# Optimization experiments

Hardware: AMD Instinct MI355X
Metric: run time of the kernel (lower is better)

## Reference

```python
import jax, jax.numpy as jnp
import numpy as np

B, D, G, K, U = 8192, 4096, 256, 32, 64


def setup_inputs() -> dict:
    key = jax.random.key(0)
    kx, kw, ki = jax.random.split(key, 3)
    x = jax.random.normal(kx, (B, D), dtype=jnp.float32)
    # per-group kernels stacked: group g has kernel [K, U]
    kernels = jax.random.normal(kw, (G, K, U), dtype=jnp.float32) * 0.02
    bias = jnp.zeros((U,), dtype=jnp.float32)
    # uniform-size index groups (TF version: list of G index lists of len K)
    indices = jax.random.randint(ki, (G, K), 0, D, dtype=jnp.int32)
    return {"x": x, "kernels": kernels, "bias": bias, "indices": indices}


def reference(x, kernels, bias, indices):
    # gather feature subsets for every group at once: [B, G, K]
    sel = x[:, indices]
    # grouped small matmuls, concatenated on group axis: [B, G, U]
    out = jnp.einsum('bgk,gku->bgu', sel, kernels)
    out = out + bias  # bias broadcast over last axis (tf.nn.bias_add)
    return jax.nn.relu(out)
```

## Files before the change

kernel.cpp:

```cpp
#include <hip/hip_runtime.h>
#include <hip/hip_bf16.h>


#define B_ 8192
#define D_ 4096
#define G_ 256
#define K_ 32
#define U_ 64
#define QG 8

typedef short v8s __attribute__((ext_vector_type(8)));
typedef float f32x4 __attribute__((ext_vector_type(4)));

__device__ __forceinline__ unsigned short f2bf(float f) {
    unsigned int u = __float_as_uint(f);
    u = (u + 0x7FFFu + ((u >> 16) & 1u)) >> 16;
    return (unsigned short)u;
}

__global__ void prep_kb(const float* __restrict__ kern, unsigned short* __restrict__ kb) {
    int tid = blockIdx.x * blockDim.x + threadIdx.x;
    if (tid >= G_ * K_ * U_) return;
    int u = tid & (U_ - 1);
    int k = (tid >> 6) & (K_ - 1);
    int g = tid >> 11;
    int t = u & 3;
    int col = u >> 2;
    int lane = ((k >> 3) << 4) | col;
    int j = k & 7;
    kb[((((g << 2) + t) << 6 | lane) << 3) | j] = f2bf(kern[tid]);
}

#define XS 4100

__global__ void __launch_bounds__(512) sdense(
        const float* __restrict__ x, const unsigned short* __restrict__ kb,
        const float* __restrict__ bias, const int* __restrict__ idx,
        float* __restrict__ out) {
    extern __shared__ unsigned short lx[];
    const int tid = threadIdx.x;
    const int b0 = blockIdx.x << 4;
    const int lane = tid & 63;
    const int w = tid >> 6;

    {
        const int row = (w << 1) + (lane >> 5);
        const int l32 = lane & 31;
        const float* xr = x + (size_t)(b0 + row) * D_;
        unsigned short* lr = lx + row * XS;
        #pragma unroll
        for (int i = 0; i < 16; ++i) {
            int col = (i << 8) + (l32 << 3);
            float4 v0 = *(const float4*)(xr + col);
            float4 v1 = *(const float4*)(xr + col + 4);
            union { unsigned short u[8]; v8s v; } st;
            st.u[0] = f2bf(v0.x); st.u[1] = f2bf(v0.y);
            st.u[2] = f2bf(v0.z); st.u[3] = f2bf(v0.w);
            st.u[4] = f2bf(v1.x); st.u[5] = f2bf(v1.y);
            st.u[6] = f2bf(v1.z); st.u[7] = f2bf(v1.w);
            *(v8s*)(lr + col) = st.v;
        }
    }
    __syncthreads();

    const int grp = lane >> 4;
    const int l15 = lane & 15;
    const int rowb = l15 * XS;
    const int kk0 = grp << 3;

    const float4 bias_v = *(const float4*)(bias + (l15 << 2));

    const v8s* kbv = (const v8s*)kb;

    for (int q = 0; q < 4; ++q) {
        const int g0 = (q << 6) + (w << 3);

        f32x4 acc[QG][4];
        #pragma unroll
        for (int j = 0; j < QG; ++j) {
            const int g = g0 + j;
            const int4* ip = (const int4*)(idx + (g << 5) + kk0);
            int4 ia = ip[0], ib = ip[1];
            const v8s* kg = kbv + (g << 8) + lane;
            v8s k0 = kg[0], k1 = kg[64], k2 = kg[128], k3 = kg[192];

            union { unsigned short u[8]; v8s v; } A;
            A.u[0] = lx[rowb + ia.x]; A.u[1] = lx[rowb + ia.y];
            A.u[2] = lx[rowb + ia.z]; A.u[3] = lx[rowb + ia.w];
            A.u[4] = lx[rowb + ib.x]; A.u[5] = lx[rowb + ib.y];
            A.u[6] = lx[rowb + ib.z]; A.u[7] = lx[rowb + ib.w];

            f32x4 z = {0.f, 0.f, 0.f, 0.f};
            acc[j][0] = __builtin_amdgcn_mfma_f32_16x16x32_bf16(A.v, k0, z, 0, 0, 0);
            acc[j][1] = __builtin_amdgcn_mfma_f32_16x16x32_bf16(A.v, k1, z, 0, 0, 0);
            acc[j][2] = __builtin_amdgcn_mfma_f32_16x16x32_bf16(A.v, k2, z, 0, 0, 0);
            acc[j][3] = __builtin_amdgcn_mfma_f32_16x16x32_bf16(A.v, k3, z, 0, 0, 0);
        }

        #pragma unroll
        for (int r = 0; r < 4; ++r) {
            float* obr = out + (size_t)(b0 + (grp << 2) + r) * (G_ * U_)
                             + (g0 << 6) + (l15 << 2);
            #pragma unroll
            for (int j = 0; j < QG; ++j) {
                float4 v;
                v.x = acc[j][0][r] + bias_v.x;
                v.y = acc[j][1][r] + bias_v.y;
                v.z = acc[j][2][r] + bias_v.z;
                v.w = acc[j][3][r] + bias_v.w;
                v.x = v.x > 0.f ? v.x : 0.f;
                v.y = v.y > 0.f ? v.y : 0.f;
                v.z = v.z > 0.f ? v.z : 0.f;
                v.w = v.w > 0.f ? v.w : 0.f;
                *(float4*)(obr + (j << 6)) = v;
            }
        }

        __builtin_amdgcn_s_barrier();
    }
}

extern "C" void kernel_launch(void* const* d_in, const int* in_sizes, int n_in,
                              void* d_out, int out_size, void* d_ws, size_t ws_size,
                              hipStream_t stream) {
    const float* x    = (const float*)d_in[0];
    const float* kern = (const float*)d_in[1];
    const float* bias = (const float*)d_in[2];
    const int*   idx  = (const int*)d_in[3];
    float* out = (float*)d_out;
    unsigned short* kb = (unsigned short*)d_ws;

    prep_kb<<<(G_ * K_ * U_ + 255) / 256, 256, 0, stream>>>(kern, kb);
    sdense<<<B_ / 16, 512, 16 * XS * sizeof(unsigned short), stream>>>(x, kb, bias, idx, out);
}
```

Baseline: 169.9 us.

## Double-buffer kernel/index loads, process two row tiles per block with swizzled mapping

```diff
diff --git a/kernel.cpp b/kernel.cpp
--- a/kernel.cpp
+++ b/kernel.cpp
@@ -7,7 +7,7 @@
 #define G_ 256
 #define K_ 32
 #define U_ 64
-#define QG 8
+#define QG 4
 
 typedef short v8s __attribute__((ext_vector_type(8)));
 typedef float f32x4 __attribute__((ext_vector_type(4)));
@@ -33,90 +33,109 @@
 
 #define XS 4100
 
+#define LOADS(BANK, G0)                                                   \
+    _Pragma("unroll")                                                     \
+    for (int j = 0; j < QG; ++j) {                                        \
+        const int4* ip = (const int4*)(idx + (((G0) + j) << 5) + kk0);    \
+        pia[BANK][j] = ip[0]; pib[BANK][j] = ip[1];                       \
+        const v8s* kg = kbv + (((G0) + j) << 8) + lane;                   \
+        pk[BANK][j][0] = kg[0];   pk[BANK][j][1] = kg[64];                \
+        pk[BANK][j][2] = kg[128]; pk[BANK][j][3] = kg[192];               \
+    }
+
+#define STEP(CB, NB, Q)                                                   \
+    {                                                                     \
+        const int g0 = ((Q) << 5) + (w << 2);                             \
+               \
+        LOADS(NB, (((((Q) + 1) & 7) << 5) + (w << 2)));                   \
+        f32x4 acc[QG][4];                                                 \
+        _Pragma("unroll")                                                 \
+        for (int j = 0; j < QG; ++j) {                                    \
+            union { unsigned short u[8]; v8s v; } A;                      \
+            A.u[0] = lx[rowb + pia[CB][j].x];                             \
+            A.u[1] = lx[rowb + pia[CB][j].y];                             \
+            A.u[2] = lx[rowb + pia[CB][j].z];                             \
+            A.u[3] = lx[rowb + pia[CB][j].w];                             \
+            A.u[4] = lx[rowb + pib[CB][j].x];                             \
+            A.u[5] = lx[rowb + pib[CB][j].y];                             \
+            A.u[6] = lx[rowb + pib[CB][j].z];                             \
+            A.u[7] = lx[rowb + pib[CB][j].w];                             \
+            f32x4 z = {0.f, 0.f, 0.f, 0.f};                               \
+            acc[j][0] = __builtin_amdgcn_mfma_f32_16x16x32_bf16(A.v, pk[CB][j][0], z, 0, 0, 0); \
+            acc[j][1] = __builtin_amdgcn_mfma_f32_16x16x32_bf16(A.v, pk[CB][j][1], z, 0, 0, 0); \
+            acc[j][2] = __builtin_amdgcn_mfma_f32_16x16x32_bf16(A.v, pk[CB][j][2], z, 0, 0, 0); \
+            acc[j][3] = __builtin_amdgcn_mfma_f32_16x16x32_bf16(A.v, pk[CB][j][3], z, 0, 0, 0); \
+        }                                                                 \
+        _Pragma("unroll")                                                 \
+        for (int r = 0; r < 4; ++r) {                                     \
+            float* obr = out + (size_t)(b0 + (grp << 2) + r) * (G_ * U_)  \
+                             + (g0 << 6) + (l15 << 2);                    \
+            _Pragma("unroll")                                             \
+            for (int j = 0; j < QG; ++j) {                                \
+                float4 v;                                                 \
+                v.x = acc[j][0][r] + bias_v.x;                            \
+                v.y = acc[j][1][r] + bias_v.y;                            \
+                v.z = acc[j][2][r] + bias_v.z;                            \
+                v.w = acc[j][3][r] + bias_v.w;                            \
+                v.x = v.x > 0.f ? v.x : 0.f;                              \
+                v.y = v.y > 0.f ? v.y : 0.f;                              \
+                v.z = v.z > 0.f ? v.z : 0.f;                              \
+                v.w = v.w > 0.f ? v.w : 0.f;                              \
+                *(float4*)(obr + (j << 6)) = v;                           \
+            }                                                             \
+        }                                                                 \
+        __builtin_amdgcn_s_barrier();                                     \
+    }
+
 __global__ void __launch_bounds__(512) sdense(
         const float* __restrict__ x, const unsigned short* __restrict__ kb,
         const float* __restrict__ bias, const int* __restrict__ idx,
         float* __restrict__ out) {
     extern __shared__ unsigned short lx[];
     const int tid = threadIdx.x;
-    const int b0 = blockIdx.x << 4;
     const int lane = tid & 63;
     const int w = tid >> 6;
-
-    {
-        const int row = (w << 1) + (lane >> 5);
-        const int l32 = lane & 31;
-        const float* xr = x + (size_t)(b0 + row) * D_;
-        unsigned short* lr = lx + row * XS;
-        #pragma unroll
-        for (int i = 0; i < 16; ++i) {
-            int col = (i << 8) + (l32 << 3);
-            float4 v0 = *(const float4*)(xr + col);
-            float4 v1 = *(const float4*)(xr + col + 4);
-            union { unsigned short u[8]; v8s v; } st;
-            st.u[0] = f2bf(v0.x); st.u[1] = f2bf(v0.y);
-            st.u[2] = f2bf(v0.z); st.u[3] = f2bf(v0.w);
-            st.u[4] = f2bf(v1.x); st.u[5] = f2bf(v1.y);
-            st.u[6] = f2bf(v1.z); st.u[7] = f2bf(v1.w);
-            *(v8s*)(lr + col) = st.v;
-        }
-    }
-    __syncthreads();
+    const int tile = ((blockIdx.x & 7) << 5) | (blockIdx.x >> 3);
 
     const int grp = lane >> 4;
     const int l15 = lane & 15;
     const int rowb = l15 * XS;
     const int kk0 = grp << 3;
-
     const float4 bias_v = *(const float4*)(bias + (l15 << 2));
-
     const v8s* kbv = (const v8s*)kb;
 
-    for (int q = 0; q < 4; ++q) {
-        const int g0 = (q << 6) + (w << 3);
+    int4 pia[2][QG], pib[2][QG];
+    v8s pk[2][QG][4];
 
-        f32x4 acc[QG][4];
-        #pragma unroll
-        for (int j = 0; j < QG; ++j) {
-            const int g = g0 + j;
-            const int4* ip = (const int4*)(idx + (g << 5) + kk0);
-            int4 ia = ip[0], ib = ip[1];
-            const v8s* kg = kbv + (g << 8) + lane;
-            v8s k0 = kg[0], k1 = kg[64], k2 = kg[128], k3 = kg[192];
+    for (int tt = 0; tt < 2; ++tt) {
+        const int b0 = (((tile << 1) + tt) << 4);
+        if (tt) __syncthreads();
 
-            union { unsigned short u[8]; v8s v; } A;
-            A.u[0] = lx[rowb + ia.x]; A.u[1] = lx[rowb + ia.y];
-            A.u[2] = lx[rowb + ia.z]; A.u[3] = lx[rowb + ia.w];
-            A.u[4] = lx[rowb + ib.x]; A.u[5] = lx[rowb + ib.y];
-            A.u[6] = lx[rowb + ib.z]; A.u[7] = lx[rowb + ib.w];
-
-            f32x4 z = {0.f, 0.f, 0.f, 0.f};
-            acc[j][0] = __builtin_amdgcn_mfma_f32_16x16x32_bf16(A.v, k0, z, 0, 0, 0);
-            acc[j][1] = __builtin_amdgcn_mfma_f32_16x16x32_bf16(A.v, k1, z, 0, 0, 0);
-            acc[j][2] = __builtin_amdgcn_mfma_f32_16x16x32_bf16(A.v, k2, z, 0, 0, 0);
-            acc[j][3] = __builtin_amdgcn_mfma_f32_16x16x32_bf16(A.v, k3, z, 0, 0, 0);
-        }
-
-        #pragma unroll
-        for (int r = 0; r < 4; ++r) {
-            float* obr = out + (size_t)(b0 + (grp << 2) + r) * (G_ * U_)
-                             + (g0 << 6) + (l15 << 2);
+        {
+            const int row = (w << 1) + (lane >> 5);
+            const int l32 = lane & 31;
+            const float* xr = x + (size_t)(b0 + row) * D_;
+            unsigned short* lr = lx + row * XS;
             #pragma unroll
-            for (int j = 0; j < QG; ++j) {
-                float4 v;
-                v.x = acc[j][0][r] + bias_v.x;
-                v.y = acc[j][1][r] + bias_v.y;
-                v.z = acc[j][2][r] + bias_v.z;
-                v.w = acc[j][3][r] + bias_v.w;
-                v.x = v.x > 0.f ? v.x : 0.f;
-                v.y = v.y > 0.f ? v.y : 0.f;
-                v.z = v.z > 0.f ? v.z : 0.f;
-                v.w = v.w > 0.f ? v.w : 0.f;
-                *(float4*)(obr + (j << 6)) = v;
+            for (int i = 0; i < 16; ++i) {
+                int col = (i << 8) + (l32 << 3);
+                float4 v0 = *(const float4*)(xr + col);
+                float4 v1 = *(const float4*)(xr + col + 4);
+                union { unsigned short u[8]; v8s v; } st;
+                st.u[0] = f2bf(v0.x); st.u[1] = f2bf(v0.y);
+                st.u[2] = f2bf(v0.z); st.u[3] = f2bf(v0.w);
+                st.u[4] = f2bf(v1.x); st.u[5] = f2bf(v1.y);
+                st.u[6] = f2bf(v1.z); st.u[7] = f2bf(v1.w);
+                *(v8s*)(lr + col) = st.v;
             }
         }
+        __syncthreads();
 
-        __builtin_amdgcn_s_barrier();
+        LOADS(0, (w << 2));
+        for (int q2 = 0; q2 < 8; q2 += 2) {
+            STEP(0, 1, q2);
+            STEP(1, 0, q2 + 1);
+        }
     }
 }
 
@@ -131,5 +150,5 @@
     unsigned short* kb = (unsigned short*)d_ws;
 
     prep_kb<<<(G_ * K_ * U_ + 255) / 256, 256, 0, stream>>>(kern, kb);
-    sdense<<<B_ / 16, 512, 16 * XS * sizeof(unsigned short), stream>>>(x, kb, bias, idx, out);
+    sdense<<<B_ / 32, 512, 16 * XS * sizeof(unsigned short), stream>>>(x, kb, bias, idx, out);
 }
```

Measured after the change: 190.7 us. +12.3%, slower.

## Halve rows per block, stage output through LDS, software-prefetch indices and weights

Applied to the files above, without the earlier changes.

```diff
diff --git a/kernel.cpp b/kernel.cpp
--- a/kernel.cpp
+++ b/kernel.cpp
@@ -7,7 +7,11 @@
 #define G_ 256
 #define K_ 32
 #define U_ 64
-#define QG 8
+#define ROWS 8
+#define WIN 32
+#define GPW 4
+#define OBS 2048
+#define XS 4100
 
 typedef short v8s __attribute__((ext_vector_type(8)));
 typedef float f32x4 __attribute__((ext_vector_type(4)));
@@ -31,26 +35,23 @@
     kb[((((g << 2) + t) << 6 | lane) << 3) | j] = f2bf(kern[tid]);
 }
 
-#define XS 4100
-
 __global__ void __launch_bounds__(512) sdense(
         const float* __restrict__ x, const unsigned short* __restrict__ kb,
         const float* __restrict__ bias, const int* __restrict__ idx,
         float* __restrict__ out) {
     extern __shared__ unsigned short lx[];
+    float* ob = (float*)(lx + ROWS * XS);
     const int tid = threadIdx.x;
-    const int b0 = blockIdx.x << 4;
     const int lane = tid & 63;
     const int w = tid >> 6;
+    const int b0 = blockIdx.x << 3;
 
     {
-        const int row = (w << 1) + (lane >> 5);
-        const int l32 = lane & 31;
-        const float* xr = x + (size_t)(b0 + row) * D_;
-        unsigned short* lr = lx + row * XS;
+        const float* xr = x + (size_t)(b0 + w) * D_;
+        unsigned short* lr = lx + w * XS;
         #pragma unroll
-        for (int i = 0; i < 16; ++i) {
-            int col = (i << 8) + (l32 << 3);
+        for (int i = 0; i < 8; ++i) {
+            int col = (i << 9) + (lane << 3);
             float4 v0 = *(const float4*)(xr + col);
             float4 v1 = *(const float4*)(xr + col + 4);
             union { unsigned short u[8]; v8s v; } st;
@@ -65,57 +66,89 @@
 
     const int grp = lane >> 4;
     const int l15 = lane & 15;
-    const int rowb = l15 * XS;
+    const int rowb = (l15 & 7) * XS;
     const int kk0 = grp << 3;
-
     const float4 bias_v = *(const float4*)(bias + (l15 << 2));
-
     const v8s* kbv = (const v8s*)kb;
 
-    for (int q = 0; q < 4; ++q) {
-        const int g0 = (q << 6) + (w << 3);
+    int4 pia[2][GPW], pib[2][GPW];
+    v8s kf[GPW][4];
 
-        f32x4 acc[QG][4];
+    #pragma unroll
+    for (int j = 0; j < GPW; ++j) {
+        const int g = (w << 2) + j;
+        const int4* ip = (const int4*)(idx + (g << 5) + kk0);
+        pia[0][j] = ip[0]; pib[0][j] = ip[1];
+        const v8s* kg = kbv + (g << 8) + lane;
+        kf[j][0] = kg[0]; kf[j][1] = kg[64]; kf[j][2] = kg[128]; kf[j][3] = kg[192];
+    }
+
+    for (int q = 0; q < 8; ++q) {
+        const int cb = q & 1, nb = cb ^ 1;
+        const int qn = (q + 1) & 7;
+
         #pragma unroll
-        for (int j = 0; j < QG; ++j) {
-            const int g = g0 + j;
+        for (int j = 0; j < GPW; ++j) {
+            const int g = (qn << 5) + (w << 2) + j;
             const int4* ip = (const int4*)(idx + (g << 5) + kk0);
-            int4 ia = ip[0], ib = ip[1];
-            const v8s* kg = kbv + (g << 8) + lane;
-            v8s k0 = kg[0], k1 = kg[64], k2 = kg[128], k3 = kg[192];
+            pia[nb][j] = ip[0]; pib[nb][j] = ip[1];
+        }
 
+        f32x4 acc[GPW][4];
+        #pragma unroll
+        for (int j = 0; j < GPW; ++j) {
             union { unsigned short u[8]; v8s v; } A;
-            A.u[0] = lx[rowb + ia.x]; A.u[1] = lx[rowb + ia.y];
-            A.u[2] = lx[rowb + ia.z]; A.u[3] = lx[rowb + ia.w];
-            A.u[4] = lx[rowb + ib.x]; A.u[5] = lx[rowb + ib.y];
-            A.u[6] = lx[rowb + ib.z]; A.u[7] = lx[rowb + ib.w];
-
+            A.u[0] = lx[rowb + pia[cb][j].x]; A.u[1] = lx[rowb + pia[cb][j].y];
+            A.u[2] = lx[rowb + pia[cb][j].z]; A.u[3] = lx[rowb + pia[cb][j].w];
+            A.u[4] = lx[rowb + pib[cb][j].x]; A.u[5] = lx[rowb + pib[cb][j].y];
+            A.u[6] = lx[rowb + pib[cb][j].z]; A.u[7] = lx[rowb + pib[cb][j].w];
             f32x4 z = {0.f, 0.f, 0.f, 0.f};
-            acc[j][0] = __builtin_amdgcn_mfma_f32_16x16x32_bf16(A.v, k0, z, 0, 0, 0);
-            acc[j][1] = __builtin_amdgcn_mfma_f32_16x16x32_bf16(A.v, k1, z, 0, 0, 0);
-            acc[j][2] = __builtin_amdgcn_mfma_f32_16x16x32_bf16(A.v, k2, z, 0, 0, 0);
-            acc[j][3] = __builtin_amdgcn_mfma_f32_16x16x32_bf16(A.v, k3, z, 0, 0, 0);
+            acc[j][0] = __builtin_amdgcn_mfma_f32_16x16x32_bf16(A.v, kf[j][0], z, 0, 0, 0);
+            acc[j][1] = __builtin_amdgcn_mfma_f32_16x16x32_bf16(A.v, kf[j][1], z, 0, 0, 0);
+            acc[j][2] = __builtin_amdgcn_mfma_f32_16x16x32_bf16(A.v, kf[j][2], z, 0, 0, 0);
+            acc[j][3] = __builtin_amdgcn_mfma_f32_16x16x32_bf16(A.v, kf[j][3], z, 0, 0, 0);
         }
 
         #pragma unroll
-        for (int r = 0; r < 4; ++r) {
-            float* obr = out + (size_t)(b0 + (grp << 2) + r) * (G_ * U_)
-                             + (g0 << 6) + (l15 << 2);
+        for (int j = 0; j < GPW; ++j) {
+            const int g = (qn << 5) + (w << 2) + j;
+            const v8s* kg = kbv + (g << 8) + lane;
+            kf[j][0] = kg[0]; kf[j][1] = kg[64]; kf[j][2] = kg[128]; kf[j][3] = kg[192];
+        }
+
+        if (grp < 2) {
             #pragma unroll
-            for (int j = 0; j < QG; ++j) {
-                float4 v;
-                v.x = acc[j][0][r] + bias_v.x;
-                v.y = acc[j][1][r] + bias_v.y;
-                v.z = acc[j][2][r] + bias_v.z;
-                v.w = acc[j][3][r] + bias_v.w;
-                v.x = v.x > 0.f ? v.x : 0.f;
-                v.y = v.y > 0.f ? v.y : 0.f;
-                v.z = v.z > 0.f ? v.z : 0.f;
-                v.w = v.w > 0.f ? v.w : 0.f;
-                *(float4*)(obr + (j << 6)) = v;
+            for (int j = 0; j < GPW; ++j) {
+                const int gl = (w << 2) + j;
+                #pragma unroll
+                for (int r = 0; r < 4; ++r) {
+                    float4 v;
+                    v.x = acc[j][0][r] + bias_v.x;
+                    v.y = acc[j][1][r] + bias_v.y;
+                    v.z = acc[j][2][r] + bias_v.z;
+                    v.w = acc[j][3][r] + bias_v.w;
+                    v.x = v.x > 0.f ? v.x : 0.f;
+                    v.y = v.y > 0.f ? v.y : 0.f;
+                    v.z = v.z > 0.f ? v.z : 0.f;
+                    v.w = v.w > 0.f ? v.w : 0.f;
+                    *(float4*)(ob + ((grp << 2) + r) * OBS + (gl << 6) + (l15 << 2)) = v;
+                }
             }
         }
+        asm volatile("s_waitcnt lgkmcnt(0)" ::: "memory");
+        __builtin_amdgcn_sched_barrier(0);
+        __builtin_amdgcn_s_barrier();
 
+        {
+            const size_t outoff = (size_t)(q << 11) + (w << 8) + (lane << 2);
+            #pragma unroll
+            for (int r = 0; r < ROWS; ++r) {
+                float4 v = *(const float4*)(ob + r * OBS + (w << 8) + (lane << 2));
+                *(float4*)(out + (size_t)(b0 + r) * (G_ * U_) + outoff) = v;
+            }
+        }
+        asm volatile("s_waitcnt lgkmcnt(0)" ::: "memory");
+        __builtin_amdgcn_sched_barrier(0);
         __builtin_amdgcn_s_barrier();
     }
 }
@@ -131,5 +164,6 @@
     unsigned short* kb = (unsigned short*)d_ws;
 
     prep_kb<<<(G_ * K_ * U_ + 255) / 256, 256, 0, stream>>>(kern, kb);
-    sdense<<<B_ / 16, 512, 16 * XS * sizeof(unsigned short), stream>>>(x, kb, bias, idx, out);
+    size_t lds = ROWS * XS * sizeof(unsigned short) + ROWS * OBS * sizeof(float);
+    sdense<<<B_ / ROWS, 512, lds, stream>>>(x, kb, bias, idx, out);
 }
```

Result: slower. 312.9 us (+84.2%).
